# Kernel tuning notes

Hardware: AMD Instinct MI355X
Metric: run time of the kernel (lower is better)

## Reference

```python
import jax, jax.numpy as jnp
import numpy as np

DIM = 1024
NUM_HEADS = 16
HEAD_DIM = DIM // NUM_HEADS
MLP_HIDDEN = 4 * DIM
SCALE = HEAD_DIM ** -0.5
EPS = 1e-5


def setup_inputs() -> dict:
    key = jax.random.key(0)
    ks = jax.random.split(key, 6)
    s = (2.0 / DIM) ** 0.5
    sd = (2.0 / MLP_HIDDEN) ** 0.5
    return {
        "x": jax.random.normal(ks[0], (2, 2048, DIM), dtype=jnp.float32),
        "attn_qkv_weight": jax.random.normal(ks[1], (3 * DIM, DIM), dtype=jnp.float32) * s,
        "attn_out_weight": jax.random.normal(ks[2], (DIM, DIM), dtype=jnp.float32) * s,
        "norm1_weight": jnp.ones((DIM,), jnp.float32),
        "norm1_bias": jnp.zeros((DIM,), jnp.float32),
        "mlp_gate_weight": jax.random.normal(ks[3], (MLP_HIDDEN, DIM), dtype=jnp.float32) * s,
        "mlp_up_weight": jax.random.normal(ks[4], (MLP_HIDDEN, DIM), dtype=jnp.float32) * s,
        "mlp_down_weight": jax.random.normal(ks[5], (DIM, MLP_HIDDEN), dtype=jnp.float32) * sd,
        "norm2_weight": jnp.ones((DIM,), jnp.float32),
        "norm2_bias": jnp.zeros((DIM,), jnp.float32),
    }


def _layer_norm(x, w, b):
    mean = x.mean(axis=-1, keepdims=True)
    var = jnp.mean(jnp.square(x - mean), axis=-1, keepdims=True)
    return (x - mean) / jnp.sqrt(var + EPS) * w + b


def reference(x, attn_qkv_weight, attn_out_weight, norm1_weight, norm1_bias,
              mlp_gate_weight, mlp_up_weight, mlp_down_weight, norm2_weight, norm2_bias):
    B, S, D = x.shape
    residual1 = x
    xn = _layer_norm(x, norm1_weight, norm1_bias)
    qkv = xn @ attn_qkv_weight.T                      # [B,S,3D]
    qkv = qkv.reshape(B, S, 3, NUM_HEADS, HEAD_DIM).transpose(2, 0, 3, 1, 4)
    q, k, v = qkv[0], qkv[1], qkv[2]                  # [B,H,S,hd]
    scores = jnp.einsum('bhqd,bhkd->bhqk', q, k) * SCALE  # full O(S^2) matrix
    attn = jax.nn.softmax(scores, axis=-1)            # no causal mask (default False)
    out = jnp.einsum('bhqk,bhkd->bhqd', attn, v)      # [B,H,S,hd]
    out = out.transpose(0, 2, 1, 3).reshape(B, S, D)
    x2 = residual1 + out @ attn_out_weight.T
    xn2 = _layer_norm(x2, norm2_weight, norm2_bias)
    gate = xn2 @ mlp_gate_weight.T
    up = xn2 @ mlp_up_weight.T
    hidden = jax.nn.silu(gate) * up
    return x2 + hidden @ mlp_down_weight.T
```

## Files before the change

kernel.cpp:

```cpp
#include <hip/hip_runtime.h>

typedef float f32x4 __attribute__((ext_vector_type(4)));
typedef __bf16 bf16x8 __attribute__((ext_vector_type(8)));
typedef unsigned int u32;

#define DEV __device__ __forceinline__

DEV void gload_lds16(const void* g, void* l) {
  __builtin_amdgcn_global_load_lds(
      (const __attribute__((address_space(1))) u32*)g,
      (__attribute__((address_space(3))) u32*)l, 16, 0, 0);
}

__global__ __launch_bounds__(256) void cvt_bf16(const float* __restrict__ in,
                                                __bf16* __restrict__ o, int n) {
  int i = (blockIdx.x * 256 + threadIdx.x) * 8;
  if (i >= n) return;
  float4 a = *(const float4*)(in + i);
  float4 b = *(const float4*)(in + i + 4);
  union { bf16x8 v; __bf16 e[8]; } u;
  u.e[0] = (__bf16)a.x; u.e[1] = (__bf16)a.y; u.e[2] = (__bf16)a.z; u.e[3] = (__bf16)a.w;
  u.e[4] = (__bf16)b.x; u.e[5] = (__bf16)b.y; u.e[6] = (__bf16)b.z; u.e[7] = (__bf16)b.w;
  *(bf16x8*)(o + i) = u.v;
}

__global__ __launch_bounds__(256) void ln_kernel(const float* __restrict__ x,
                                                 const float* __restrict__ w,
                                                 const float* __restrict__ b,
                                                 __bf16* __restrict__ o) {
  const int row = blockIdx.x, tid = threadIdx.x;
  const float4 v = ((const float4*)(x + (size_t)row * 1024))[tid];
  float s  = v.x + v.y + v.z + v.w;
  float s2 = v.x * v.x + v.y * v.y + v.z * v.z + v.w * v.w;
  for (int off = 32; off; off >>= 1) {
    s  += __shfl_down(s, off);
    s2 += __shfl_down(s2, off);
  }
  __shared__ float rs[4], rs2[4];
  if ((tid & 63) == 0) { rs[tid >> 6] = s; rs2[tid >> 6] = s2; }
  __syncthreads();
  float S = rs[0] + rs[1] + rs[2] + rs[3];
  float S2 = rs2[0] + rs2[1] + rs2[2] + rs2[3];
  float mean = S * (1.0f / 1024.0f);
  float var = S2 * (1.0f / 1024.0f) - mean * mean;
  float inv = rsqrtf(var + 1e-5f);
  const float4 wv = ((const float4*)w)[tid];
  const float4 bv = ((const float4*)b)[tid];
  union { ushort4 u4; __bf16 e[4]; } u;
  u.e[0] = (__bf16)((v.x - mean) * inv * wv.x + bv.x);
  u.e[1] = (__bf16)((v.y - mean) * inv * wv.y + bv.y);
  u.e[2] = (__bf16)((v.z - mean) * inv * wv.z + bv.z);
  u.e[3] = (__bf16)((v.w - mean) * inv * wv.w + bv.w);
  *(ushort4*)(o + (size_t)row * 1024 + tid * 4) = u.u4;
}

template <int EPI, int MI>
__global__ __launch_bounds__(256) void gemm_bt(const __bf16* __restrict__ A,
                                               const __bf16* __restrict__ B,
                                               void* __restrict__ Cout,
                                               const float* __restrict__ Res,
                                               int M, int N, int K) {
  constexpr int BM = MI * 32;
  __shared__ __align__(16) __bf16 As[BM * 32];
  __shared__ __align__(16) __bf16 Bs[128 * 32];
  const int tid = threadIdx.x;
  const int lane = tid & 63;
  const int w = tid >> 6;
  const int wr = w >> 1, wc = w & 1;
  const int l15 = lane & 15, g = lane >> 4;
  const int bm = blockIdx.y * BM, bn = blockIdx.x * 128;

  f32x4 acc[MI][4] = {};

  for (int k0 = 0; k0 < K; k0 += 32) {
#pragma unroll
    for (int p = 0; p < MI / 2; ++p) {
      const int ch = p * 256 + tid;
      const int row = ch >> 2, c = ch & 3;
      gload_lds16(A + (size_t)(bm + row) * K + k0 + c * 8, As + (p * 256 + w * 64) * 8);
    }
#pragma unroll
    for (int p = 0; p < 2; ++p) {
      const int ch = p * 256 + tid;
      const int row = ch >> 2, c = ch & 3;
      gload_lds16(B + (size_t)(bn + row) * K + k0 + c * 8, Bs + (p * 256 + w * 64) * 8);
    }
    asm volatile("s_waitcnt vmcnt(0)" ::: "memory");
    __syncthreads();
    bf16x8 af[MI], bfr[4];
#pragma unroll
    for (int i = 0; i < MI; ++i)
      af[i] = *(const bf16x8*)(As + (wr * (MI * 16) + i * 16 + l15) * 32 + g * 8);
#pragma unroll
    for (int j = 0; j < 4; ++j)
      bfr[j] = *(const bf16x8*)(Bs + (wc * 64 + j * 16 + l15) * 32 + g * 8);
#pragma unroll
    for (int i = 0; i < MI; ++i)
#pragma unroll
      for (int j = 0; j < 4; ++j)
        acc[i][j] = __builtin_amdgcn_mfma_f32_16x16x32_bf16(af[i], bfr[j], acc[i][j], 0, 0, 0);
    __syncthreads();
  }

  const int r0 = bm + wr * (MI * 16) + g * 4;
  const int c0 = bn + wc * 64 + l15;
#pragma unroll
  for (int i = 0; i < MI; ++i)
#pragma unroll
    for (int j = 0; j < 4; ++j)
#pragma unroll
      for (int r = 0; r < 4; ++r) {
        const size_t idx = (size_t)(r0 + i * 16 + r) * N + (c0 + j * 16);
        const float v = acc[i][j][r];
        if (EPI == 0) {
          ((__bf16*)Cout)[idx] = (__bf16)v;
        } else if (EPI == 1) {
          ((float*)Cout)[idx] = v + Res[idx];
        } else {
          __bf16* C = (__bf16*)Cout;
          const float gt = (float)C[idx];
          const float sg = gt / (1.0f + __expf(-gt));
          C[idx] = (__bf16)(sg * v);
        }
      }
}

__global__ __launch_bounds__(256) void transpose_v(const __bf16* __restrict__ qkv,
                                                   __bf16* __restrict__ vT) {
  const int st = blockIdx.x, bh = blockIdx.y;
  const int b = bh >> 4, h = bh & 15;
  __shared__ __bf16 tile[64][80];
  const int tid = threadIdx.x;
#pragma unroll
  for (int it = 0; it < 2; ++it) {
    const int idx = it * 256 + tid;
    const int r = idx >> 3, c0 = (idx & 7) * 8;
    bf16x8 v = *(const bf16x8*)(qkv + (size_t)(b * 2048 + st * 64 + r) * 3072 + 2048 + h * 64 + c0);
    *(bf16x8*)&tile[r][c0] = v;
  }
  __syncthreads();
#pragma unroll
  for (int it = 0; it < 2; ++it) {
    const int idx = it * 256 + tid;
    const int d = idx >> 3, s0 = (idx & 7) * 8;
    union { bf16x8 v; __bf16 e[8]; } u;
#pragma unroll
    for (int j = 0; j < 8; ++j) u.e[j] = tile[s0 + j][d];
    *(bf16x8*)(vT + (size_t)(bh * 64 + d) * 2048 + st * 64 + s0) = u.v;
  }
}

__global__ __launch_bounds__(256) void attn_kernel(const __bf16* __restrict__ qkv,
                                                   const __bf16* __restrict__ vT,
                                                   __bf16* __restrict__ outp) {
  const int qt = blockIdx.x, bh = blockIdx.y;
  const int b = bh >> 4, h = bh & 15;
  const int tid = threadIdx.x, lane = tid & 63, w = tid >> 6;
  const int l15 = lane & 15, g = lane >> 4;
  const float CSC = 0.125f * 1.44269504f;

  __shared__ __align__(16) __bf16 Ks[64 * 64];
  __shared__ __align__(16) __bf16 Vs[64 * 64];
  __shared__ __align__(16) __bf16 Ps[4][16 * 80];

  const int qrow = qt * 64 + w * 16 + l15;
  const size_t qbase = (size_t)(b * 2048 + qrow) * 3072 + h * 64;
  const bf16x8 qf0 = *(const bf16x8*)(qkv + qbase + g * 8);
  const bf16x8 qf1 = *(const bf16x8*)(qkv + qbase + 32 + g * 8);

  f32x4 o_acc[4] = {};
  float l_r[4] = {0.f, 0.f, 0.f, 0.f};

  const size_t kgbase = (size_t)(b * 2048) * 3072 + 1024 + h * 64;
  const size_t vgbase = (size_t)bh * 64 * 2048;

  for (int t = 0; t < 32; ++t) {
    const int kv0 = t * 64;
#pragma unroll
    for (int p = 0; p < 2; ++p) {
      const int ch = p * 256 + w * 64 + lane;
      const int row = ch >> 3, c = ch & 7;
      const int gc = c ^ (row & 7);
      gload_lds16(qkv + kgbase + (size_t)(kv0 + row) * 3072 + gc * 8, Ks + (p * 256 + w * 64) * 8);
      gload_lds16(vT + vgbase + (size_t)row * 2048 + kv0 + gc * 8, Vs + (p * 256 + w * 64) * 8);
    }
    asm volatile("s_waitcnt vmcnt(0)" ::: "memory");
    __syncthreads();

    f32x4 sf[4];
    __builtin_amdgcn_s_setprio(1);
#pragma unroll
    for (int ni = 0; ni < 4; ++ni) {
      const int krow = ni * 16 + l15;
      const __bf16* kb = Ks + krow * 64;
      const bf16x8 kf0 = *(const bf16x8*)(kb + ((g ^ (krow & 7)) * 8));
      const bf16x8 kf1 = *(const bf16x8*)(kb + (((4 + g) ^ (krow & 7)) * 8));
      f32x4 z = {0.f, 0.f, 0.f, 0.f};
      z = __builtin_amdgcn_mfma_f32_16x16x32_bf16(qf0, kf0, z, 0, 0, 0);
      z = __builtin_amdgcn_mfma_f32_16x16x32_bf16(qf1, kf1, z, 0, 0, 0);
      sf[ni] = z;
    }
    __builtin_amdgcn_s_setprio(0);

#pragma unroll
    for (int ni = 0; ni < 4; ++ni)
#pragma unroll
      for (int r = 0; r < 4; ++r) {
        const float pv = exp2f(sf[ni][r] * CSC);
        sf[ni][r] = pv;
        l_r[r] += pv;
      }

    __bf16* pw = Ps[w];
#pragma unroll
    for (int ni = 0; ni < 4; ++ni)
#pragma unroll
      for (int r = 0; r < 4; ++r) {
        const int row = g * 4 + r;
        const int pc = (ni * 2 + (l15 >> 3)) ^ (row & 7);
        pw[row * 80 + pc * 8 + (l15 & 7)] = (__bf16)sf[ni][r];
      }
    asm volatile("" ::: "memory");
    const bf16x8 pa0 = *(const bf16x8*)(pw + l15 * 80 + ((g ^ (l15 & 7)) * 8));
    const bf16x8 pa1 = *(const bf16x8*)(pw + l15 * 80 + (((4 + g) ^ (l15 & 7)) * 8));

    __builtin_amdgcn_s_setprio(1);
#pragma unroll
    for (int ni = 0; ni < 4; ++ni) {
      const int vrow = ni * 16 + l15;
      const __bf16* vb = Vs + vrow * 64;
      const bf16x8 vf0 = *(const bf16x8*)(vb + ((g ^ (vrow & 7)) * 8));
      const bf16x8 vf1 = *(const bf16x8*)(vb + (((4 + g) ^ (vrow & 7)) * 8));
      o_acc[ni] = __builtin_amdgcn_mfma_f32_16x16x32_bf16(pa0, vf0, o_acc[ni], 0, 0, 0);
      o_acc[ni] = __builtin_amdgcn_mfma_f32_16x16x32_bf16(pa1, vf1, o_acc[ni], 0, 0, 0);
    }
    __builtin_amdgcn_s_setprio(0);
    __syncthreads();
  }

#pragma unroll
  for (int mk = 1; mk < 16; mk <<= 1)
#pragma unroll
    for (int r = 0; r < 4; ++r) l_r[r] += __shfl_xor(l_r[r], mk);
#pragma unroll
  for (int r = 0; r < 4; ++r) {
    const int orow = qt * 64 + w * 16 + g * 4 + r;
    const float invl = 1.0f / l_r[r];
#pragma unroll
    for (int ni = 0; ni < 4; ++ni)
      outp[(size_t)(b * 2048 + orow) * 1024 + h * 64 + ni * 16 + l15] =
          (__bf16)(o_acc[ni][r] * invl);
  }
}

extern "C" void kernel_launch(void* const* d_in, const int* in_sizes, int n_in,
                              void* d_out, int out_size, void* d_ws, size_t ws_size,
                              hipStream_t stream) {
  const float* x     = (const float*)d_in[0];
  const float* Wqkv  = (const float*)d_in[1];
  const float* Wout  = (const float*)d_in[2];
  const float* n1w   = (const float*)d_in[3];
  const float* n1b   = (const float*)d_in[4];
  const float* Wgate = (const float*)d_in[5];
  const float* Wup   = (const float*)d_in[6];
  const float* Wdown = (const float*)d_in[7];
  const float* n2w   = (const float*)d_in[8];
  const float* n2b   = (const float*)d_in[9];
  float* out = (float*)d_out;
  char* ws = (char*)d_ws;
  const size_t MB = 1u << 20;

  __bf16* XN  = (__bf16*)(ws + 0);
  __bf16* QKV = (__bf16*)(ws + 8 * MB);
  __bf16* VT  = (__bf16*)(ws + 32 * MB);
  __bf16* ATT = (__bf16*)(ws + 40 * MB);
  float*  X2  = (float*)(ws + 48 * MB);
  __bf16* G   = QKV;
  __bf16* WQ  = (__bf16*)(ws + 64 * MB);
  __bf16* WO  = (__bf16*)(ws + 70 * MB);
  __bf16* WG  = (__bf16*)(ws + 72 * MB);
  __bf16* WU  = (__bf16*)(ws + 80 * MB);
  __bf16* WD  = (__bf16*)(ws + 88 * MB);

  cvt_bf16<<<3145728 / 2048, 256, 0, stream>>>(Wqkv, WQ, 3145728);
  cvt_bf16<<<1048576 / 2048, 256, 0, stream>>>(Wout, WO, 1048576);
  cvt_bf16<<<4194304 / 2048, 256, 0, stream>>>(Wgate, WG, 4194304);
  cvt_bf16<<<4194304 / 2048, 256, 0, stream>>>(Wup, WU, 4194304);
  cvt_bf16<<<4194304 / 2048, 256, 0, stream>>>(Wdown, WD, 4194304);

  ln_kernel<<<4096, 256, 0, stream>>>(x, n1w, n1b, XN);
  gemm_bt<0, 4><<<dim3(24, 32), 256, 0, stream>>>(XN, WQ, QKV, nullptr, 4096, 3072, 1024);
  transpose_v<<<dim3(32, 32), 256, 0, stream>>>(QKV, VT);
  attn_kernel<<<dim3(32, 32), 256, 0, stream>>>(QKV, VT, ATT);
  gemm_bt<1, 2><<<dim3(8, 64), 256, 0, stream>>>(ATT, WO, X2, x, 4096, 1024, 1024);
  ln_kernel<<<4096, 256, 0, stream>>>(X2, n2w, n2b, XN);
  gemm_bt<0, 4><<<dim3(32, 32), 256, 0, stream>>>(XN, WG, G, nullptr, 4096, 4096, 1024);
  gemm_bt<2, 4><<<dim3(32, 32), 256, 0, stream>>>(XN, WU, G, nullptr, 4096, 4096, 1024);
  gemm_bt<1, 2><<<dim3(8, 64), 256, 0, stream>>>(G, WD, out, X2, 4096, 1024, 4096);

  (void)in_sizes; (void)n_in; (void)out_size; (void)ws_size;
}
```

Baseline: 382.7 us.

## Double-buffer GEMM LDS, fuse gate/up GEMMs, add XCD-aware block swizzle

The GEMM kernel now double-buffers its LDS tiles so the next K-slice loads while MFMAs run on the current one, and drops one barrier per iteration. The gate and up projections are merged into a single kernel that shares the A tile and applies SiLU-multiply in registers. This avoids writing the gate result to memory and reading it back. Block indices in the GEMMs and in attention are remapped so that neighbouring tiles land on the same XCD, which should improve L2 reuse. The fused kernel holds two accumulator sets and uses larger LDS buffers, so register pressure rises and occupancy may drop.

```diff
diff --git a/kernel.cpp b/kernel.cpp
--- a/kernel.cpp
+++ b/kernel.cpp
@@ -10,6 +10,10 @@
   __builtin_amdgcn_global_load_lds(
       (const __attribute__((address_space(1))) u32*)g,
       (__attribute__((address_space(3))) u32*)l, 16, 0, 0);
+}
+
+DEV int xcd_swz(int flat, int nwg) {
+  return (flat & 7) * (nwg >> 3) + (flat >> 3);
 }
 
 __global__ __launch_bounds__(256) void cvt_bf16(const float* __restrict__ in,
@@ -61,45 +65,60 @@
                                                const float* __restrict__ Res,
                                                int M, int N, int K) {
   constexpr int BM = MI * 32;
-  __shared__ __align__(16) __bf16 As[BM * 32];
-  __shared__ __align__(16) __bf16 Bs[128 * 32];
+  __shared__ __align__(16) __bf16 As[2][BM * 32];
+  __shared__ __align__(16) __bf16 Bs[2][128 * 32];
   const int tid = threadIdx.x;
   const int lane = tid & 63;
   const int w = tid >> 6;
   const int wr = w >> 1, wc = w & 1;
   const int l15 = lane & 15, g = lane >> 4;
-  const int bm = blockIdx.y * BM, bn = blockIdx.x * 128;
+
+  const int nbx = gridDim.x;
+  const int logical = xcd_swz(blockIdx.y * nbx + blockIdx.x, nbx * gridDim.y);
+  const int bm = (logical / nbx) * BM, bn = (logical % nbx) * 128;
 
   f32x4 acc[MI][4] = {};
 
-  for (int k0 = 0; k0 < K; k0 += 32) {
+  auto stage = [&](int buf, int k0) {
 #pragma unroll
     for (int p = 0; p < MI / 2; ++p) {
       const int ch = p * 256 + tid;
       const int row = ch >> 2, c = ch & 3;
-      gload_lds16(A + (size_t)(bm + row) * K + k0 + c * 8, As + (p * 256 + w * 64) * 8);
+      gload_lds16(A + (size_t)(bm + row) * K + k0 + c * 8, &As[buf][(p * 256 + w * 64) * 8]);
     }
 #pragma unroll
     for (int p = 0; p < 2; ++p) {
       const int ch = p * 256 + tid;
       const int row = ch >> 2, c = ch & 3;
-      gload_lds16(B + (size_t)(bn + row) * K + k0 + c * 8, Bs + (p * 256 + w * 64) * 8);
-    }
+      gload_lds16(B + (size_t)(bn + row) * K + k0 + c * 8, &Bs[buf][(p * 256 + w * 64) * 8]);
+    }
+  };
+
+  stage(0, 0);
+  asm volatile("s_waitcnt vmcnt(0)" ::: "memory");
+  __syncthreads();
+
+  int cur = 0;
+  for (int k0 = 0;;) {
+    const int nk = k0 + 32;
+    if (nk < K) stage(cur ^ 1, nk);
+    bf16x8 af[MI], bfr[4];
+#pragma unroll
+    for (int i = 0; i < MI; ++i)
+      af[i] = *(const bf16x8*)(&As[cur][(wr * (MI * 16) + i * 16 + l15) * 32 + g * 8]);
+#pragma unroll
+    for (int j = 0; j < 4; ++j)
+      bfr[j] = *(const bf16x8*)(&Bs[cur][(wc * 64 + j * 16 + l15) * 32 + g * 8]);
+#pragma unroll
+    for (int i = 0; i < MI; ++i)
+#pragma unroll
+      for (int j = 0; j < 4; ++j)
+        acc[i][j] = __builtin_amdgcn_mfma_f32_16x16x32_bf16(af[i], bfr[j], acc[i][j], 0, 0, 0);
+    if (nk >= K) break;
     asm volatile("s_waitcnt vmcnt(0)" ::: "memory");
     __syncthreads();
-    bf16x8 af[MI], bfr[4];
-#pragma unroll
-    for (int i = 0; i < MI; ++i)
-      af[i] = *(const bf16x8*)(As + (wr * (MI * 16) + i * 16 + l15) * 32 + g * 8);
-#pragma unroll
-    for (int j = 0; j < 4; ++j)
-      bfr[j] = *(const bf16x8*)(Bs + (wc * 64 + j * 16 + l15) * 32 + g * 8);
-#pragma unroll
-    for (int i = 0; i < MI; ++i)
-#pragma unroll
-      for (int j = 0; j < 4; ++j)
-        acc[i][j] = __builtin_amdgcn_mfma_f32_16x16x32_bf16(af[i], bfr[j], acc[i][j], 0, 0, 0);
-    __syncthreads();
+    cur ^= 1;
+    k0 = nk;
   }
 
   const int r0 = bm + wr * (MI * 16) + g * 4;
@@ -112,16 +131,87 @@
       for (int r = 0; r < 4; ++r) {
         const size_t idx = (size_t)(r0 + i * 16 + r) * N + (c0 + j * 16);
         const float v = acc[i][j][r];
-        if (EPI == 0) {
-          ((__bf16*)Cout)[idx] = (__bf16)v;
-        } else if (EPI == 1) {
-          ((float*)Cout)[idx] = v + Res[idx];
-        } else {
-          __bf16* C = (__bf16*)Cout;
-          const float gt = (float)C[idx];
-          const float sg = gt / (1.0f + __expf(-gt));
-          C[idx] = (__bf16)(sg * v);
-        }
+        if (EPI == 0) ((__bf16*)Cout)[idx] = (__bf16)v;
+        else          ((float*)Cout)[idx] = v + Res[idx];
+      }
+}
+
+__global__ __launch_bounds__(256, 2) void gemm_mlp(const __bf16* __restrict__ A,
+                                                   const __bf16* __restrict__ BG,
+                                                   const __bf16* __restrict__ BU,
+                                                   __bf16* __restrict__ H,
+                                                   int M, int N, int K) {
+  __shared__ __align__(16) __bf16 As[2][128 * 32];
+  __shared__ __align__(16) __bf16 Bg[2][128 * 32];
+  __shared__ __align__(16) __bf16 Bu[2][128 * 32];
+  const int tid = threadIdx.x;
+  const int lane = tid & 63;
+  const int w = tid >> 6;
+  const int wr = w >> 1, wc = w & 1;
+  const int l15 = lane & 15, g = lane >> 4;
+
+  const int nbx = gridDim.x;
+  const int logical = xcd_swz(blockIdx.y * nbx + blockIdx.x, nbx * gridDim.y);
+  const int bm = (logical / nbx) * 128, bn = (logical % nbx) * 128;
+
+  f32x4 accg[4][4] = {};
+  f32x4 accu[4][4] = {};
+
+  auto stage = [&](int buf, int k0) {
+#pragma unroll
+    for (int p = 0; p < 2; ++p) {
+      const int ch = p * 256 + tid;
+      const int row = ch >> 2, c = ch & 3;
+      const int dst = (p * 256 + w * 64) * 8;
+      gload_lds16(A + (size_t)(bm + row) * K + k0 + c * 8, &As[buf][dst]);
+      gload_lds16(BG + (size_t)(bn + row) * K + k0 + c * 8, &Bg[buf][dst]);
+      gload_lds16(BU + (size_t)(bn + row) * K + k0 + c * 8, &Bu[buf][dst]);
+    }
+  };
+
+  stage(0, 0);
+  asm volatile("s_waitcnt vmcnt(0)" ::: "memory");
+  __syncthreads();
+
+  int cur = 0;
+  for (int k0 = 0;;) {
+    const int nk = k0 + 32;
+    if (nk < K) stage(cur ^ 1, nk);
+    bf16x8 af[4], bgf[4], buf_[4];
+#pragma unroll
+    for (int i = 0; i < 4; ++i)
+      af[i] = *(const bf16x8*)(&As[cur][(wr * 64 + i * 16 + l15) * 32 + g * 8]);
+#pragma unroll
+    for (int j = 0; j < 4; ++j) {
+      bgf[j] = *(const bf16x8*)(&Bg[cur][(wc * 64 + j * 16 + l15) * 32 + g * 8]);
+      buf_[j] = *(const bf16x8*)(&Bu[cur][(wc * 64 + j * 16 + l15) * 32 + g * 8]);
+    }
+#pragma unroll
+    for (int i = 0; i < 4; ++i)
+#pragma unroll
+      for (int j = 0; j < 4; ++j) {
+        accg[i][j] = __builtin_amdgcn_mfma_f32_16x16x32_bf16(af[i], bgf[j], accg[i][j], 0, 0, 0);
+        accu[i][j] = __builtin_amdgcn_mfma_f32_16x16x32_bf16(af[i], buf_[j], accu[i][j], 0, 0, 0);
+      }
+    if (nk >= K) break;
+    asm volatile("s_waitcnt vmcnt(0)" ::: "memory");
+    __syncthreads();
+    cur ^= 1;
+    k0 = nk;
+  }
+
+  const int r0 = bm + wr * 64 + g * 4;
+  const int c0 = bn + wc * 64 + l15;
+#pragma unroll
+  for (int i = 0; i < 4; ++i)
+#pragma unroll
+    for (int j = 0; j < 4; ++j)
+#pragma unroll
+      for (int r = 0; r < 4; ++r) {
+        const float gt = accg[i][j][r];
+        const float ut = accu[i][j][r];
+        const float h = gt / (1.0f + __expf(-gt)) * ut;
+        H[(size_t)(r0 + i * 16 + r) * N + (c0 + j * 16)] = (__bf16)h;
       }
 }
 
@@ -153,7 +243,8 @@
 __global__ __launch_bounds__(256) void attn_kernel(const __bf16* __restrict__ qkv,
                                                    const __bf16* __restrict__ vT,
                                                    __bf16* __restrict__ outp) {
-  const int qt = blockIdx.x, bh = blockIdx.y;
+  const int logical = xcd_swz(blockIdx.y * 32 + blockIdx.x, 1024);
+  const int qt = logical & 31, bh = logical >> 5;
   const int b = bh >> 4, h = bh & 15;
   const int tid = threadIdx.x, lane = tid & 63, w = tid >> 6;
   const int l15 = lane & 15, g = lane >> 4;
@@ -275,7 +366,7 @@
   __bf16* VT  = (__bf16*)(ws + 32 * MB);
   __bf16* ATT = (__bf16*)(ws + 40 * MB);
   float*  X2  = (float*)(ws + 48 * MB);
-  __bf16* G   = QKV;
+  __bf16* H   = QKV;
   __bf16* WQ  = (__bf16*)(ws + 64 * MB);
   __bf16* WO  = (__bf16*)(ws + 70 * MB);
   __bf16* WG  = (__bf16*)(ws + 72 * MB);
@@ -294,9 +385,8 @@
   attn_kernel<<<dim3(32, 32), 256, 0, stream>>>(QKV, VT, ATT);
   gemm_bt<1, 2><<<dim3(8, 64), 256, 0, stream>>>(ATT, WO, X2, x, 4096, 1024, 1024);
   ln_kernel<<<4096, 256, 0, stream>>>(X2, n2w, n2b, XN);
-  gemm_bt<0, 4><<<dim3(32, 32), 256, 0, stream>>>(XN, WG, G, nullptr, 4096, 4096, 1024);
-  gemm_bt<2, 4><<<dim3(32, 32), 256, 0, stream>>>(XN, WU, G, nullptr, 4096, 4096, 1024);
-  gemm_bt<1, 2><<<dim3(8, 64), 256, 0, stream>>>(G, WD, out, X2, 4096, 1024, 4096);
+  gemm_mlp<<<dim3(32, 32), 256, 0, stream>>>(XN, WG, WU, H, 4096, 4096, 1024);
+  gemm_bt<1, 2><<<dim3(8, 64), 256, 0, stream>>>(H, WD, out, X2, 4096, 1024, 4096);
 
   (void)in_sizes; (void)n_in; (void)out_size; (void)ws_size;
 }
```

Measured after the change: 355.3 us. 1.08x faster.
